# Optimization experiments

Hardware: AMD Instinct MI355X
Metric: run time of the kernel (lower is better)

Reference implementation:

```python
import jax, jax.numpy as jnp
import numpy as np

POS_THRESH = 0.5

def cxcy_to_xy(cxcy):
    return jnp.concatenate([cxcy[..., :2] - cxcy[..., 2:] / 2,
                            cxcy[..., :2] + cxcy[..., 2:] / 2], axis=-1)

def xy_to_cxcy(xy):
    return jnp.concatenate([(xy[..., :2] + xy[..., 2:]) / 2,
                            xy[..., 2:] - xy[..., :2]], axis=-1)

def iou_matrix(a, b):
    # a: [A,4] corner boxes, b: [N,4] corner boxes -> [A,N]
    lt = jnp.maximum(a[:, None, :2], b[None, :, :2])
    rb = jnp.minimum(a[:, None, 2:], b[None, :, 2:])
    wh = jnp.clip(rb - lt, 0.0)
    inter = wh[..., 0] * wh[..., 1]
    area_a = (a[:, 2] - a[:, 0]) * (a[:, 3] - a[:, 1])
    area_b = (b[:, 2] - b[:, 0]) * (b[:, 3] - b[:, 1])
    return inter / (area_a[:, None] + area_b[None, :] - inter)

def encode(gt_cxcy, anc_cxcy):
    # standard SSD variance encoding
    g_cxcy = (gt_cxcy[:, :2] - anc_cxcy[:, :2]) / (anc_cxcy[:, 2:] / 10.0)
    g_wh = jnp.log(gt_cxcy[:, 2:] / anc_cxcy[:, 2:]) * 5.0
    return jnp.concatenate([g_cxcy, g_wh], axis=1)

def setup_inputs() -> dict:
    key = jax.random.key(0)
    k1, k2, k3, k4, k5 = jax.random.split(key, 5)
    B, N, A = 64, 64, 24564
    # valid gt corner boxes in [0,1]
    gc = jax.random.uniform(k1, (B, N, 2), minval=0.2, maxval=0.8)
    gwh = jax.random.uniform(k2, (B, N, 2), minval=0.05, maxval=0.3)
    gt_boxes = jnp.concatenate([gc - gwh / 2, gc + gwh / 2], axis=-1)
    gt_labels = jax.random.randint(k3, (B, N), 0, 20)
    ac = jax.random.uniform(k4, (A, 2), minval=0.05, maxval=0.95)
    awh = jax.random.uniform(k5, (A, 2), minval=0.03, maxval=0.5)
    center_anchor = jnp.concatenate([ac, awh], axis=-1)
    return {"gt_boxes": gt_boxes, "gt_labels": gt_labels, "center_anchor": center_anchor}

def _match_one(boxes, labels, center_anchor, corner_anchor):
    # boxes:[N,4] corner, labels:[N], anchors:[A,4]
    N = boxes.shape[0]
    iou = iou_matrix(corner_anchor, boxes)            # [A,N]
    obj_idx = jnp.argmax(iou, axis=0)                 # best anchor per object [N]
    iou = iou.at[obj_idx, jnp.arange(N)].set(1.0)     # force-match
    positive = jnp.any(iou >= POS_THRESH, axis=1)     # [A] bool
    max_anchors_idx = jnp.argmax(iou, axis=1)         # best object per anchor [A]
    classes = (labels[max_anchors_idx] + 1) * positive.astype(labels.dtype)
    gt_center = xy_to_cxcy(boxes[max_anchors_idx])    # [A,4]
    locations = encode(gt_center, center_anchor)      # [A,4]
    return classes, locations, positive

def reference(gt_boxes, gt_labels, center_anchor):
    corner_anchor = cxcy_to_xy(center_anchor)
    gt_classes, gt_locations, gt_masks = jax.vmap(
        lambda b, l: _match_one(b, l, center_anchor, corner_anchor)
    )(gt_boxes, gt_labels)
    return gt_classes, gt_locations, gt_masks
```

## Files before the change

kernel.cpp:

```cpp
#include <hip/hip_runtime.h>
#include <hip/hip_bf16.h>


#define NOBJ 64
#define SPLITK 4

__global__ void k_init(const float4* __restrict__ gt_boxes,
                       unsigned long long* __restrict__ keys,
                       float* __restrict__ areas, int BN) {
#pragma clang fp contract(off)
    int i = blockIdx.x * blockDim.x + threadIdx.x;
    if (i < BN) {
        keys[i] = 0ull;
        float4 bx = gt_boxes[i];
        areas[i] = (bx.z - bx.x) * (bx.w - bx.y);
    }
}

__global__ __launch_bounds__(256) void k_best_anchor(
    const float4* __restrict__ gt_boxes,
    const float4* __restrict__ center_anchor,
    unsigned long long* __restrict__ keys,
    int A, int N)
{
#pragma clang fp contract(off)
    const int b    = blockIdx.y;
    const int wv   = threadIdx.x >> 6;
    const int lane = threadIdx.x & 63;
    const int job  = blockIdx.x * 4 + wv;
    const int pair = job >> 2;
    const int spl  = job & (SPLITK - 1);
    const int n0   = pair * 2, n1 = n0 + 1;

    const int Q   = (A + SPLITK - 1) / SPLITK;
    const int beg = spl * Q;
    const int end = min(A, beg + Q);

    const float4 B0 = gt_boxes[b * N + n0];
    const float4 B1 = gt_boxes[b * N + n1];
    const float ar0 = (B0.z - B0.x) * (B0.w - B0.y);
    const float ar1 = (B1.z - B1.x) * (B1.w - B1.y);

    float bv0 = -1.0f, bv1 = -1.0f;
    int   bi0 = 0,     bi1 = 0;

    for (int j = beg + lane; j < end; j += 64) {
        float4 ca = center_anchor[j];
        float hw = ca.z * 0.5f, hh = ca.w * 0.5f;
        float ax0 = ca.x - hw, ay0 = ca.y - hh;
        float ax1 = ca.x + hw, ay1 = ca.y + hh;
        float aarea = (ax1 - ax0) * (ay1 - ay0);

        {
            float ltx = fmaxf(ax0, B0.x), lty = fmaxf(ay0, B0.y);
            float rbx = fminf(ax1, B0.z), rby = fminf(ay1, B0.w);
            float wx = fmaxf(rbx - ltx, 0.0f), wy = fmaxf(rby - lty, 0.0f);
            float inter = wx * wy;
            float v = inter / ((aarea + ar0) - inter);
            if (v > bv0) { bv0 = v; bi0 = j; }
        }
        {
            float ltx = fmaxf(ax0, B1.x), lty = fmaxf(ay0, B1.y);
            float rbx = fminf(ax1, B1.z), rby = fminf(ay1, B1.w);
            float wx = fmaxf(rbx - ltx, 0.0f), wy = fmaxf(rby - lty, 0.0f);
            float inter = wx * wy;
            float v = inter / ((aarea + ar1) - inter);
            if (v > bv1) { bv1 = v; bi1 = j; }
        }
    }
    for (int m = 1; m < 64; m <<= 1) {
        float ov0 = __shfl_xor(bv0, m); int oi0 = __shfl_xor(bi0, m);
        float ov1 = __shfl_xor(bv1, m); int oi1 = __shfl_xor(bi1, m);
        if (ov0 > bv0 || (ov0 == bv0 && oi0 < bi0)) { bv0 = ov0; bi0 = oi0; }
        if (ov1 > bv1 || (ov1 == bv1 && oi1 < bi1)) { bv1 = ov1; bi1 = oi1; }
    }
    if (lane == 0) {
        unsigned long long k0 =
            ((unsigned long long)__float_as_uint(bv0) << 32) |
            (unsigned long long)(unsigned)(~(unsigned)bi0);
        unsigned long long k1 =
            ((unsigned long long)__float_as_uint(bv1) << 32) |
            (unsigned long long)(unsigned)(~(unsigned)bi1);
        atomicMax(&keys[b * N + n0], k0);
        atomicMax(&keys[b * N + n1], k1);
    }
}

__global__ __launch_bounds__(256) void k_match(
    const float4* __restrict__ gt_boxes,
    const int*    __restrict__ gt_labels,
    const float4* __restrict__ center_anchor,
    const unsigned long long* __restrict__ keys,
    const float*  __restrict__ areas,
    float* __restrict__ out,
    int A, int N, int BA)
{
#pragma clang fp contract(off)
    __shared__ float4 sbox[NOBJ];
    __shared__ int    slab[NOBJ];
    const int b   = blockIdx.y;
    const int tid = threadIdx.x;
    const int bN  = b * N;
    if (tid < NOBJ) {
        sbox[tid] = gt_boxes[bN + tid];
        slab[tid] = gt_labels[bN + tid];
    }
    __syncthreads();

    const int a = blockIdx.x * 256 + tid;
    if (a >= A) return;

    const float4 ca = center_anchor[a];
    const float hw = ca.z * 0.5f, hh = ca.w * 0.5f;
    const float ax0 = ca.x - hw, ay0 = ca.y - hh;
    const float ax1 = ca.x + hw, ay1 = ca.y + hh;
    const float aarea = (ax1 - ax0) * (ay1 - ay0);

    float best_v = -1.0f;
    int   best_n = 0;

#pragma unroll 8
    for (int nn = 0; nn < NOBJ; ++nn) {
        const float4 bx  = gt_boxes[bN + nn];
        const float  bar = areas[bN + nn];
        const int    fid = (int)(~(unsigned)(keys[bN + nn] & 0xffffffffull));
        float ltx = fmaxf(ax0, bx.x), lty = fmaxf(ay0, bx.y);
        float rbx = fminf(ax1, bx.z), rby = fminf(ay1, bx.w);
        float wx = fmaxf(rbx - ltx, 0.0f), wy = fmaxf(rby - lty, 0.0f);
        float inter = wx * wy;
        float v = inter / ((aarea + bar) - inter);
        if (fid == a) v = 1.0f;
        if (v > best_v) { best_v = v; best_n = nn; }
    }
    const bool pos = (best_v >= 0.5f);
    const int  cls = pos ? (slab[best_n] + 1) : 0;

    const float4 gb = sbox[best_n];
    const float gcx = (gb.x + gb.z) * 0.5f;
    const float gcy = (gb.y + gb.w) * 0.5f;
    const float gw  = gb.z - gb.x;
    const float gh  = gb.w - gb.y;
    const float l0 = (gcx - ca.x) / (ca.z / 10.0f);
    const float l1 = (gcy - ca.y) / (ca.w / 10.0f);
    const float l2 = __logf(gw / ca.z) * 5.0f;
    const float l3 = __logf(gh / ca.w) * 5.0f;

    const int idx = b * A + a;
    out[idx] = (float)cls;
    reinterpret_cast<float4*>(out + (size_t)BA)[idx] =
        make_float4(l0, l1, l2, l3);
    out[(size_t)5 * BA + idx] = pos ? 1.0f : 0.0f;
}

extern "C" void kernel_launch(void* const* d_in, const int* in_sizes, int n_in,
                              void* d_out, int out_size, void* d_ws, size_t ws_size,
                              hipStream_t stream) {
    const float4* gt_boxes      = (const float4*)d_in[0];
    const int*    gt_labels     = (const int*)d_in[1];
    const float4* center_anchor = (const float4*)d_in[2];

    const int N  = NOBJ;
    const int BN = in_sizes[1];
    const int B  = BN / N;
    const int A  = in_sizes[2] / 4;
    const int BA = B * A;

    float* out = (float*)d_out;
    unsigned long long* keys = (unsigned long long*)d_ws;
    float* areas = (float*)((char*)d_ws + (size_t)BN * 8);

    k_init<<<(BN + 255) / 256, 256, 0, stream>>>(gt_boxes, keys, areas, BN);

    dim3 g1((N / 2) * SPLITK / 4, B);
    k_best_anchor<<<g1, 256, 0, stream>>>(gt_boxes, center_anchor, keys, A, N);

    dim3 g2((A + 255) / 256, B);
    k_match<<<g2, 256, 0, stream>>>(gt_boxes, gt_labels, center_anchor, keys,
                                    areas, out, A, N, BA);
}
```

Measured before the change: 224.8 us.

## Compute IoU once, fusing per-object argmax and per-anchor best into one pass

Result: faster. 193.7 us (-13.9%).

```diff
diff --git a/kernel.cpp b/kernel.cpp
--- a/kernel.cpp
+++ b/kernel.cpp
@@ -3,11 +3,163 @@
 
 
 #define NOBJ 64
+#define VEC 4
+#define FINF 0x7FFFFFFF
+
+
+__global__ void k_init_fast(const float4* __restrict__ gt_boxes,
+                            unsigned long long* __restrict__ keys,
+                            float* __restrict__ gareas,
+                            int* __restrict__ forced,
+                            int BN, int BA) {
+#pragma clang fp contract(off)
+    int i = blockIdx.x * blockDim.x + threadIdx.x;
+    if (i < BN) {
+        keys[i] = 0ull;
+        float4 bx = gt_boxes[i];
+        gareas[i] = (bx.z - bx.x) * (bx.w - bx.y);
+    }
+    if (i < BA) forced[i] = FINF;
+}
+
+__global__ __launch_bounds__(256) void k_iou(
+    const float4* __restrict__ gt_boxes,
+    const float4* __restrict__ center_anchor,
+    const float*  __restrict__ gareas,
+    unsigned long long* __restrict__ keys,
+    unsigned long long* __restrict__ pbest,
+    int A, int N)
+{
+#pragma clang fp contract(off)
+    const int b     = blockIdx.y;
+    const int wv    = threadIdx.x >> 6;
+    const int lane  = threadIdx.x & 63;
+    const int wbase = (blockIdx.x * 4 + wv) * (64 * VEC);
+    const int bN    = b * N;
+
+    float ax0[VEC], ay0[VEC], ax1[VEC], ay1[VEC], aar[VEC];
+    int   aidx[VEC];
+    bool  val[VEC];
+#pragma unroll
+    for (int v = 0; v < VEC; ++v) {
+        int a   = wbase + v * 64 + lane;
+        val[v]  = (a < A);
+        int ac  = val[v] ? a : (A - 1);
+        float4 ca = center_anchor[ac];
+        float hw = ca.z * 0.5f, hh = ca.w * 0.5f;
+        ax0[v] = ca.x - hw; ay0[v] = ca.y - hh;
+        ax1[v] = ca.x + hw; ay1[v] = ca.y + hh;
+        aar[v] = (ax1[v] - ax0[v]) * (ay1[v] - ay0[v]);
+        aidx[v] = a;
+    }
+    float bv[VEC]; int bn[VEC];
+#pragma unroll
+    for (int v = 0; v < VEC; ++v) { bv[v] = -1.0f; bn[v] = 0; }
+
+    for (int n = 0; n < NOBJ; ++n) {
+        const float4 bx  = gt_boxes[bN + n];
+        const float  bar = gareas[bN + n];
+        float mv = -1.0f; int ma = 0;
+#pragma unroll
+        for (int v = 0; v < VEC; ++v) {
+            float ltx = fmaxf(ax0[v], bx.x), lty = fmaxf(ay0[v], bx.y);
+            float rbx = fminf(ax1[v], bx.z), rby = fminf(ay1[v], bx.w);
+            float wx = fmaxf(rbx - ltx, 0.0f), wy = fmaxf(rby - lty, 0.0f);
+            float inter = wx * wy;
+            float iou = inter / ((aar[v] + bar) - inter);
+            if (val[v]) {
+                if (iou > bv[v]) { bv[v] = iou; bn[v] = n; }
+                if (iou > mv)    { mv = iou;    ma = aidx[v]; }
+            }
+        }
+        unsigned long long mk = (mv >= 0.0f)
+            ? (((unsigned long long)__float_as_uint(mv) << 32) |
+               (unsigned long long)(unsigned)(~(unsigned)ma))
+            : 0ull;
+        for (int m = 1; m < 64; m <<= 1) {
+            unsigned long long ok = __shfl_xor(mk, m);
+            if (ok > mk) mk = ok;
+        }
+        if (lane == 0 && mk != 0ull) atomicMax(&keys[bN + n], mk);
+    }
+    const long long base = (long long)b * A;
+#pragma unroll
+    for (int v = 0; v < VEC; ++v) {
+        if (val[v]) {
+            pbest[base + aidx[v]] =
+                ((unsigned long long)__float_as_uint(bv[v]) << 32) |
+                (unsigned long long)(unsigned)bn[v];
+        }
+    }
+}
+
+__global__ void k_forced(const unsigned long long* __restrict__ keys,
+                         int* __restrict__ forced, int A, int N, int BN) {
+    int i = blockIdx.x * blockDim.x + threadIdx.x;
+    if (i < BN) {
+        int b = i >> 6, n = i & 63;
+        int aidx = (int)(~(unsigned)(keys[i] & 0xffffffffull));
+        atomicMin(&forced[(long long)b * A + aidx], n);
+    }
+}
+
+__global__ __launch_bounds__(256) void k_final(
+    const float4* __restrict__ gt_boxes,
+    const int*    __restrict__ gt_labels,
+    const float4* __restrict__ center_anchor,
+    const unsigned long long* __restrict__ pbest,
+    const int*    __restrict__ forced,
+    float* __restrict__ out, int A, int N, int BA)
+{
+#pragma clang fp contract(off)
+    __shared__ float4 sbox[NOBJ];
+    __shared__ int    slab[NOBJ];
+    const int b = blockIdx.y, tid = threadIdx.x, bN = b * N;
+    if (tid < NOBJ) { sbox[tid] = gt_boxes[bN + tid]; slab[tid] = gt_labels[bN + tid]; }
+    __syncthreads();
+
+    const int a = blockIdx.x * 256 + tid;
+    if (a >= A) return;
+    const long long ia = (long long)b * A + a;
+
+    const unsigned long long pb = pbest[ia];
+    const float bv  = __uint_as_float((unsigned)(pb >> 32));
+    const int   bn  = (int)(pb & 0xffffffffull);
+    const int   fid = forced[ia];
+
+    bool pos; int best;
+    if (fid != FINF) {
+        pos  = true;
+        best = (bv == 1.0f && bn < fid) ? bn : fid;
+    } else {
+        pos  = (bv >= 0.5f);
+        best = bn;
+    }
+    const int cls = pos ? (slab[best] + 1) : 0;
+
+    const float4 ca = center_anchor[a];
+    const float4 gb = sbox[best];
+    const float gcx = (gb.x + gb.z) * 0.5f;
+    const float gcy = (gb.y + gb.w) * 0.5f;
+    const float gw  = gb.z - gb.x;
+    const float gh  = gb.w - gb.y;
+    const float l0 = (gcx - ca.x) / (ca.z / 10.0f);
+    const float l1 = (gcy - ca.y) / (ca.w / 10.0f);
+    const float l2 = __logf(gw / ca.z) * 5.0f;
+    const float l3 = __logf(gh / ca.w) * 5.0f;
+
+    const int idx = b * A + a;
+    out[idx] = (float)cls;
+    reinterpret_cast<float4*>(out + (size_t)BA)[idx] = make_float4(l0, l1, l2, l3);
+    out[(size_t)5 * BA + idx] = pos ? 1.0f : 0.0f;
+}
+
+
 #define SPLITK 4
 
-__global__ void k_init(const float4* __restrict__ gt_boxes,
-                       unsigned long long* __restrict__ keys,
-                       float* __restrict__ areas, int BN) {
+__global__ void k_init_fb(const float4* __restrict__ gt_boxes,
+                          unsigned long long* __restrict__ keys,
+                          float* __restrict__ areas, int BN) {
 #pragma clang fp contract(off)
     int i = blockIdx.x * blockDim.x + threadIdx.x;
     if (i < BN) {
@@ -20,8 +172,7 @@
 __global__ __launch_bounds__(256) void k_best_anchor(
     const float4* __restrict__ gt_boxes,
     const float4* __restrict__ center_anchor,
-    unsigned long long* __restrict__ keys,
-    int A, int N)
+    unsigned long long* __restrict__ keys, int A, int N)
 {
 #pragma clang fp contract(off)
     const int b    = blockIdx.y;
@@ -50,7 +201,6 @@
         float ax0 = ca.x - hw, ay0 = ca.y - hh;
         float ax1 = ca.x + hw, ay1 = ca.y + hh;
         float aarea = (ax1 - ax0) * (ay1 - ay0);
-
         {
             float ltx = fmaxf(ax0, B0.x), lty = fmaxf(ay0, B0.y);
             float rbx = fminf(ax1, B0.z), rby = fminf(ay1, B0.w);
@@ -92,19 +242,13 @@
     const float4* __restrict__ center_anchor,
     const unsigned long long* __restrict__ keys,
     const float*  __restrict__ areas,
-    float* __restrict__ out,
-    int A, int N, int BA)
+    float* __restrict__ out, int A, int N, int BA)
 {
 #pragma clang fp contract(off)
     __shared__ float4 sbox[NOBJ];
     __shared__ int    slab[NOBJ];
-    const int b   = blockIdx.y;
-    const int tid = threadIdx.x;
-    const int bN  = b * N;
-    if (tid < NOBJ) {
-        sbox[tid] = gt_boxes[bN + tid];
-        slab[tid] = gt_labels[bN + tid];
-    }
+    const int b = blockIdx.y, tid = threadIdx.x, bN = b * N;
+    if (tid < NOBJ) { sbox[tid] = gt_boxes[bN + tid]; slab[tid] = gt_labels[bN + tid]; }
     __syncthreads();
 
     const int a = blockIdx.x * 256 + tid;
@@ -147,10 +291,10 @@
 
     const int idx = b * A + a;
     out[idx] = (float)cls;
-    reinterpret_cast<float4*>(out + (size_t)BA)[idx] =
-        make_float4(l0, l1, l2, l3);
+    reinterpret_cast<float4*>(out + (size_t)BA)[idx] = make_float4(l0, l1, l2, l3);
     out[(size_t)5 * BA + idx] = pos ? 1.0f : 0.0f;
 }
+
 
 extern "C" void kernel_launch(void* const* d_in, const int* in_sizes, int n_in,
                               void* d_out, int out_size, void* d_ws, size_t ws_size,
@@ -164,17 +308,36 @@
     const int B  = BN / N;
     const int A  = in_sizes[2] / 4;
     const int BA = B * A;
-
     float* out = (float*)d_out;
-    unsigned long long* keys = (unsigned long long*)d_ws;
-    float* areas = (float*)((char*)d_ws + (size_t)BN * 8);
-
-    k_init<<<(BN + 255) / 256, 256, 0, stream>>>(gt_boxes, keys, areas, BN);
-
-    dim3 g1((N / 2) * SPLITK / 4, B);
-    k_best_anchor<<<g1, 256, 0, stream>>>(gt_boxes, center_anchor, keys, A, N);
-
-    dim3 g2((A + 255) / 256, B);
-    k_match<<<g2, 256, 0, stream>>>(gt_boxes, gt_labels, center_anchor, keys,
-                                    areas, out, A, N, BA);
-}
+
+    char* w = (char*)d_ws;
+    unsigned long long* keys   = (unsigned long long*)w;
+    float*              gareas = (float*)(w + (size_t)BN * 8);
+    size_t off_forced = (size_t)BN * 8 + (size_t)BN * 4;
+    off_forced = (off_forced + 7) & ~(size_t)7;
+    int*                forced = (int*)(w + off_forced);
+    size_t off_pbest = off_forced + (size_t)BA * 4;
+    off_pbest = (off_pbest + 7) & ~(size_t)7;
+    unsigned long long* pbest  = (unsigned long long*)(w + off_pbest);
+    const size_t need = off_pbest + (size_t)BA * 8;
+
+    if (ws_size >= need) {
+        k_init_fast<<<(BA + 255) / 256, 256, 0, stream>>>(gt_boxes, keys, gareas,
+                                                          forced, BN, BA);
+        const int APB = 4 * 64 * VEC;
+        dim3 g1((A + APB - 1) / APB, B);
+        k_iou<<<g1, 256, 0, stream>>>(gt_boxes, center_anchor, gareas,
+                                      keys, pbest, A, N);
+        k_forced<<<(BN + 255) / 256, 256, 0, stream>>>(keys, forced, A, N, BN);
+        dim3 g2((A + 255) / 256, B);
+        k_final<<<g2, 256, 0, stream>>>(gt_boxes, gt_labels, center_anchor,
+                                        pbest, forced, out, A, N, BA);
+    } else {
+        k_init_fb<<<(BN + 255) / 256, 256, 0, stream>>>(gt_boxes, keys, gareas, BN);
+        dim3 g1((N / 2) * SPLITK / 4, B);
+        k_best_anchor<<<g1, 256, 0, stream>>>(gt_boxes, center_anchor, keys, A, N);
+        dim3 g2((A + 255) / 256, B);
+        k_match<<<g2, 256, 0, stream>>>(gt_boxes, gt_labels, center_anchor, keys,
+                                        gareas, out, A, N, BA);
+    }
+}
```
